# Kernel tuning notes

Measured on AMD Instinct MI355X. Metric: run time of the kernel, lower is better.

## Reference

```python
import jax, jax.numpy as jnp
import numpy as np

NUM_BATCHES = 8  # number of sparse-tensor batch instances


def setup_inputs() -> dict:
    key = jax.random.key(0)
    k1, k2, k3, k4 = jax.random.split(key, 4)
    N, C, R = 262144, 256, 4
    Cr = C // R
    x_feats = jax.random.normal(k1, (N, C), dtype=jnp.float32)
    batch_ids = jax.random.randint(k2, (N,), 0, NUM_BATCHES, dtype=jnp.int32)
    # MinkowskiLinear params (kaiming-ish scale)
    W1 = jax.random.normal(k3, (C, Cr), dtype=jnp.float32) * (1.0 / np.sqrt(C))
    b1 = jnp.zeros((Cr,), dtype=jnp.float32)
    W2 = jax.random.normal(k4, (Cr, C), dtype=jnp.float32) * (1.0 / np.sqrt(Cr))
    b2 = jnp.zeros((C,), dtype=jnp.float32)
    return {"x_feats": x_feats, "batch_ids": batch_ids, "W1": W1, "b1": b1, "W2": W2, "b2": b2}


def reference(x_feats, batch_ids, W1, b1, W2, b2):
    # MinkowskiGlobalPooling: per-batch average over irregular point sets -> [B, C]
    sums = jax.ops.segment_sum(x_feats, batch_ids, num_segments=NUM_BATCHES)
    counts = jax.ops.segment_sum(jnp.ones((x_feats.shape[0],), x_feats.dtype),
                                 batch_ids, num_segments=NUM_BATCHES)
    pooled = sums / jnp.maximum(counts, 1.0)[:, None]  # [B, C]
    # Squeeze-excite MLP: Linear -> ReLU -> Linear -> Sigmoid
    h = jax.nn.relu(pooled @ W1 + b1)                  # [B, C/r]
    y = jax.nn.sigmoid(h @ W2 + b2)                    # [B, C]
    # Broadcast excitation back to each sparse point and multiply
    return y[batch_ids] * x_feats                      # [N, C]
```

## Files before the change

kernel.cpp:

```cpp
#include <hip/hip_runtime.h>
#include <math.h>

#define NB 8
#define C  256
#define CR 64

#define POOL_BLOCKS  1024
#define SCALE_BLOCKS 2048

typedef float vf4 __attribute__((ext_vector_type(4)));

__global__ __launch_bounds__(256) void pool_kernel(
    const float* __restrict__ x,
    const int*   __restrict__ bids,
    float*       __restrict__ partials,
    float*       __restrict__ cpart,
    int N)
{
    __shared__ float lsum[4][NB][C];
    __shared__ float lcnt[4][NB];

    const int tid  = threadIdx.x;
    const int wid  = tid >> 6;
    const int lane = tid & 63;

    vf4   acc[NB];
    float cnt[NB];
    #pragma unroll
    for (int b = 0; b < NB; ++b) { acc[b] = (vf4){0.f,0.f,0.f,0.f}; cnt[b] = 0.f; }

    const int gwave   = blockIdx.x * 4 + wid;
    const int totw    = POOL_BLOCKS * 4;
    const int ngroups = N >> 2;

    for (int g = gwave; g < ngroups; g += totw) {
        const size_t r0 = (size_t)g * 4;
        const int4 bb = *((const int4*)(bids + r0));
        const int b0 = __builtin_amdgcn_readfirstlane(bb.x);
        const int b1 = __builtin_amdgcn_readfirstlane(bb.y);
        const int b2 = __builtin_amdgcn_readfirstlane(bb.z);
        const int b3 = __builtin_amdgcn_readfirstlane(bb.w);
        const vf4 v0 = __builtin_nontemporal_load(((const vf4*)(x + (r0 + 0) * C)) + lane);
        const vf4 v1 = __builtin_nontemporal_load(((const vf4*)(x + (r0 + 1) * C)) + lane);
        const vf4 v2 = __builtin_nontemporal_load(((const vf4*)(x + (r0 + 2) * C)) + lane);
        const vf4 v3 = __builtin_nontemporal_load(((const vf4*)(x + (r0 + 3) * C)) + lane);
        #pragma unroll
        for (int b = 0; b < NB; ++b) {
            const float m0 = (b0 == b) ? 1.f : 0.f;
            const float m1 = (b1 == b) ? 1.f : 0.f;
            const float m2 = (b2 == b) ? 1.f : 0.f;
            const float m3 = (b3 == b) ? 1.f : 0.f;
            acc[b] += v0 * m0;
            acc[b] += v1 * m1;
            acc[b] += v2 * m2;
            acc[b] += v3 * m3;
            cnt[b] += m0 + m1 + m2 + m3;
        }
    }
    if (gwave == 0) {
        for (int row = ngroups * 4; row < N; ++row) {
            const int bb = __builtin_amdgcn_readfirstlane(bids[row]);
            const vf4 v = ((const vf4*)(x + (size_t)row * C))[lane];
            #pragma unroll
            for (int b = 0; b < NB; ++b) {
                const float m = (bb == b) ? 1.f : 0.f;
                acc[b] += v * m;
                cnt[b] += m;
            }
        }
    }

    #pragma unroll
    for (int b = 0; b < NB; ++b)
        ((vf4*)&lsum[wid][b][0])[lane] = acc[b];
    if (lane == 0) {
        #pragma unroll
        for (int b = 0; b < NB; ++b) lcnt[wid][b] = cnt[b];
    }
    __syncthreads();

    float* pout = partials + (size_t)blockIdx.x * (NB * C);
    for (int i = tid; i < NB * C; i += 256)
        pout[i] = lsum[0][0][i] + lsum[1][0][i] + lsum[2][0][i] + lsum[3][0][i];
    if (tid < NB)
        cpart[blockIdx.x * NB + tid] =
            lcnt[0][tid] + lcnt[1][tid] + lcnt[2][tid] + lcnt[3][tid];
}

__global__ __launch_bounds__(256) void reduce_kernel(
    const float* __restrict__ partials,
    const float* __restrict__ cpart,
    float*       __restrict__ partial2,
    float*       __restrict__ c2)
{
    const int jo  = blockIdx.x & 7;
    const int jp  = blockIdx.x >> 3;
    const int col = jo * 256 + threadIdx.x;
    const int PR  = POOL_BLOCKS / 8;

    float s = 0.f;
    #pragma unroll 8
    for (int p = 0; p < PR; ++p)
        s += partials[(size_t)(jp * PR + p) * (NB * C) + col];
    partial2[jp * (NB * C) + col] = s;

    if (jo == 0 && threadIdx.x < NB) {
        float c = 0.f;
        for (int p = 0; p < PR; ++p)
            c += cpart[(jp * PR + p) * NB + threadIdx.x];
        c2[jp * NB + threadIdx.x] = c;
    }
}

__global__ __launch_bounds__(256) void mlp_kernel(
    const float* __restrict__ partial2,
    const float* __restrict__ c2,
    const float* __restrict__ W1,
    const float* __restrict__ b1,
    const float* __restrict__ W2,
    const float* __restrict__ b2,
    float*       __restrict__ y)
{
    __shared__ float pooled[NB][C];
    __shared__ float h[NB][CR];
    __shared__ float cnts[NB];
    const int tid = threadIdx.x;

    if (tid < NB) {
        float c = 0.f;
        #pragma unroll
        for (int j = 0; j < 8; ++j) c += c2[j * NB + tid];
        cnts[tid] = fmaxf(c, 1.f);
    }
    __syncthreads();

    for (int i = tid; i < NB * C; i += 256) {
        float s = 0.f;
        #pragma unroll
        for (int j = 0; j < 8; ++j) s += partial2[j * (NB * C) + i];
        (&pooled[0][0])[i] = s / cnts[i >> 8];
    }
    __syncthreads();

    for (int o = tid; o < NB * CR; o += 256) {
        const int b = o >> 6, j = o & 63;
        float acc = b1[j];
        #pragma unroll 4
        for (int k = 0; k < C; ++k) acc = fmaf(pooled[b][k], W1[k * CR + j], acc);
        (&h[0][0])[o] = fmaxf(acc, 0.f);
    }
    __syncthreads();

    for (int o = tid; o < NB * C; o += 256) {
        const int b = o >> 8, j = o & 255;
        float acc = b2[j];
        #pragma unroll
        for (int k = 0; k < CR; ++k) acc = fmaf(h[b][k], W2[k * C + j], acc);
        y[o] = 1.f / (1.f + __expf(-acc));
    }
}

__global__ __launch_bounds__(256) void scale_kernel(
    const float* __restrict__ x,
    const int*   __restrict__ bids,
    const float* __restrict__ y,
    float*       __restrict__ out,
    int N)
{
    __shared__ float ly[NB][C];
    const int tid = threadIdx.x;
    for (int i = tid; i < NB * C; i += 256) (&ly[0][0])[i] = y[i];
    __syncthreads();

    const int wid  = tid >> 6;
    const int lane = tid & 63;
    const int gwave   = blockIdx.x * 4 + wid;
    const int totw    = SCALE_BLOCKS * 4;
    const int ngroups = N >> 2;

    for (int g = gwave; g < ngroups; g += totw) {
        const size_t r0 = (size_t)g * 4;
        const int4 bb = *((const int4*)(bids + r0));
        const int b0 = __builtin_amdgcn_readfirstlane(bb.x);
        const int b1 = __builtin_amdgcn_readfirstlane(bb.y);
        const int b2 = __builtin_amdgcn_readfirstlane(bb.z);
        const int b3 = __builtin_amdgcn_readfirstlane(bb.w);
        const vf4 v0 = __builtin_nontemporal_load(((const vf4*)(x + (r0 + 0) * C)) + lane);
        const vf4 v1 = __builtin_nontemporal_load(((const vf4*)(x + (r0 + 1) * C)) + lane);
        const vf4 v2 = __builtin_nontemporal_load(((const vf4*)(x + (r0 + 2) * C)) + lane);
        const vf4 v3 = __builtin_nontemporal_load(((const vf4*)(x + (r0 + 3) * C)) + lane);
        const vf4 g0 = ((const vf4*)&ly[b0][0])[lane];
        const vf4 g1 = ((const vf4*)&ly[b1][0])[lane];
        const vf4 g2 = ((const vf4*)&ly[b2][0])[lane];
        const vf4 g3 = ((const vf4*)&ly[b3][0])[lane];
        __builtin_nontemporal_store(v0 * g0, ((vf4*)(out + (r0 + 0) * C)) + lane);
        __builtin_nontemporal_store(v1 * g1, ((vf4*)(out + (r0 + 1) * C)) + lane);
        __builtin_nontemporal_store(v2 * g2, ((vf4*)(out + (r0 + 2) * C)) + lane);
        __builtin_nontemporal_store(v3 * g3, ((vf4*)(out + (r0 + 3) * C)) + lane);
    }
    if (gwave == 0) {
        for (int row = ngroups * 4; row < N; ++row) {
            const int bb = __builtin_amdgcn_readfirstlane(bids[row]);
            const vf4 v  = ((const vf4*)(x + (size_t)row * C))[lane];
            const vf4 gg = ((const vf4*)&ly[bb][0])[lane];
            ((vf4*)(out + (size_t)row * C))[lane] = v * gg;
        }
    }
}

extern "C" void kernel_launch(void* const* d_in, const int* in_sizes, int n_in,
                              void* d_out, int out_size, void* d_ws, size_t ws_size,
                              hipStream_t stream)
{
    const float* x    = (const float*)d_in[0];
    const int*   bids = (const int*)  d_in[1];
    const float* W1   = (const float*)d_in[2];
    const float* b1   = (const float*)d_in[3];
    const float* W2   = (const float*)d_in[4];
    const float* b2   = (const float*)d_in[5];
    float* out = (float*)d_out;

    const int N = in_sizes[1];

    float* partials = (float*)d_ws;
    float* cpart    = partials + POOL_BLOCKS * (NB * C);
    float* partial2 = cpart + POOL_BLOCKS * NB;
    float* c2       = partial2 + 8 * (NB * C);
    float* gy       = c2 + 64;

    pool_kernel  <<<POOL_BLOCKS, 256, 0, stream>>>(x, bids, partials, cpart, N);
    reduce_kernel<<<64, 256, 0, stream>>>(partials, cpart, partial2, c2);
    mlp_kernel   <<<1, 256, 0, stream>>>(partial2, c2, W1, b1, W2, b2, gy);
    scale_kernel <<<SCALE_BLOCKS, 256, 0, stream>>>(x, bids, gy, out, N);
}
```

Before: 169.7 us.

## Fuse partial reduction with MLP per batch, halve pool blocks, widen scale unroll

Result: slower. 174.6 us (+2.9%).

```diff
diff --git a/kernel.cpp b/kernel.cpp
--- a/kernel.cpp
+++ b/kernel.cpp
@@ -5,7 +5,7 @@
 #define C  256
 #define CR 64
 
-#define POOL_BLOCKS  1024
+#define POOL_BLOCKS  512
 #define SCALE_BLOCKS 2048
 
 typedef float vf4 __attribute__((ext_vector_type(4)));
@@ -87,76 +87,54 @@
             lcnt[0][tid] + lcnt[1][tid] + lcnt[2][tid] + lcnt[3][tid];
 }
 
-__global__ __launch_bounds__(256) void reduce_kernel(
+__global__ __launch_bounds__(256) void reduce_mlp_kernel(
     const float* __restrict__ partials,
     const float* __restrict__ cpart,
-    float*       __restrict__ partial2,
-    float*       __restrict__ c2)
-{
-    const int jo  = blockIdx.x & 7;
-    const int jp  = blockIdx.x >> 3;
-    const int col = jo * 256 + threadIdx.x;
-    const int PR  = POOL_BLOCKS / 8;
-
-    float s = 0.f;
-    #pragma unroll 8
-    for (int p = 0; p < PR; ++p)
-        s += partials[(size_t)(jp * PR + p) * (NB * C) + col];
-    partial2[jp * (NB * C) + col] = s;
-
-    if (jo == 0 && threadIdx.x < NB) {
-        float c = 0.f;
-        for (int p = 0; p < PR; ++p)
-            c += cpart[(jp * PR + p) * NB + threadIdx.x];
-        c2[jp * NB + threadIdx.x] = c;
-    }
-}
-
-__global__ __launch_bounds__(256) void mlp_kernel(
-    const float* __restrict__ partial2,
-    const float* __restrict__ c2,
     const float* __restrict__ W1,
     const float* __restrict__ b1,
     const float* __restrict__ W2,
     const float* __restrict__ b2,
     float*       __restrict__ y)
 {
-    __shared__ float pooled[NB][C];
-    __shared__ float h[NB][CR];
-    __shared__ float cnts[NB];
+    __shared__ float pooled[C];
+    __shared__ float h[CR];
+    __shared__ float red[256];
+
+    const int b   = blockIdx.x;
     const int tid = threadIdx.x;
 
-    if (tid < NB) {
-        float c = 0.f;
+    float s = 0.f;
+    #pragma unroll 8
+    for (int p = 0; p < POOL_BLOCKS; ++p)
+        s += partials[(size_t)p * (NB * C) + b * C + tid];
+
+    float c = 0.f;
+    for (int p = tid; p < POOL_BLOCKS; p += 256) c += cpart[p * NB + b];
+    red[tid] = c;
+    __syncthreads();
+    #pragma unroll
+    for (int off = 128; off > 0; off >>= 1) {
+        if (tid < off) red[tid] += red[tid + off];
+        __syncthreads();
+    }
+    const float cnt = fmaxf(red[0], 1.f);
+
+    pooled[tid] = s / cnt;
+    __syncthreads();
+
+    if (tid < CR) {
+        float a = b1[tid];
+        #pragma unroll 4
+        for (int k = 0; k < C; ++k) a = fmaf(pooled[k], W1[k * CR + tid], a);
+        h[tid] = fmaxf(a, 0.f);
+    }
+    __syncthreads();
+
+    {
+        float a = b2[tid];
         #pragma unroll
-        for (int j = 0; j < 8; ++j) c += c2[j * NB + tid];
-        cnts[tid] = fmaxf(c, 1.f);
-    }
-    __syncthreads();
-
-    for (int i = tid; i < NB * C; i += 256) {
-        float s = 0.f;
-        #pragma unroll
-        for (int j = 0; j < 8; ++j) s += partial2[j * (NB * C) + i];
-        (&pooled[0][0])[i] = s / cnts[i >> 8];
-    }
-    __syncthreads();
-
-    for (int o = tid; o < NB * CR; o += 256) {
-        const int b = o >> 6, j = o & 63;
-        float acc = b1[j];
-        #pragma unroll 4
-        for (int k = 0; k < C; ++k) acc = fmaf(pooled[b][k], W1[k * CR + j], acc);
-        (&h[0][0])[o] = fmaxf(acc, 0.f);
-    }
-    __syncthreads();
-
-    for (int o = tid; o < NB * C; o += 256) {
-        const int b = o >> 8, j = o & 255;
-        float acc = b2[j];
-        #pragma unroll
-        for (int k = 0; k < CR; ++k) acc = fmaf(h[b][k], W2[k * C + j], acc);
-        y[o] = 1.f / (1.f + __expf(-acc));
+        for (int k = 0; k < CR; ++k) a = fmaf(h[k], W2[k * C + tid], a);
+        y[b * C + tid] = 1.f / (1.f + __expf(-a));
     }
 }
 
@@ -174,32 +152,49 @@
 
     const int wid  = tid >> 6;
     const int lane = tid & 63;
-    const int gwave   = blockIdx.x * 4 + wid;
-    const int totw    = SCALE_BLOCKS * 4;
-    const int ngroups = N >> 2;
-
-    for (int g = gwave; g < ngroups; g += totw) {
-        const size_t r0 = (size_t)g * 4;
-        const int4 bb = *((const int4*)(bids + r0));
-        const int b0 = __builtin_amdgcn_readfirstlane(bb.x);
-        const int b1 = __builtin_amdgcn_readfirstlane(bb.y);
-        const int b2 = __builtin_amdgcn_readfirstlane(bb.z);
-        const int b3 = __builtin_amdgcn_readfirstlane(bb.w);
+    const int gwave    = blockIdx.x * 4 + wid;
+    const int totw     = SCALE_BLOCKS * 4;
+    const int ngroups8 = N >> 3;
+
+    for (int g = gwave; g < ngroups8; g += totw) {
+        const size_t r0 = (size_t)g * 8;
+        const int4 ba = *((const int4*)(bids + r0));
+        const int4 bc = *((const int4*)(bids + r0 + 4));
+        const int b0 = __builtin_amdgcn_readfirstlane(ba.x);
+        const int b1 = __builtin_amdgcn_readfirstlane(ba.y);
+        const int b2 = __builtin_amdgcn_readfirstlane(ba.z);
+        const int b3 = __builtin_amdgcn_readfirstlane(ba.w);
+        const int b4 = __builtin_amdgcn_readfirstlane(bc.x);
+        const int b5 = __builtin_amdgcn_readfirstlane(bc.y);
+        const int b6 = __builtin_amdgcn_readfirstlane(bc.z);
+        const int b7 = __builtin_amdgcn_readfirstlane(bc.w);
         const vf4 v0 = __builtin_nontemporal_load(((const vf4*)(x + (r0 + 0) * C)) + lane);
         const vf4 v1 = __builtin_nontemporal_load(((const vf4*)(x + (r0 + 1) * C)) + lane);
         const vf4 v2 = __builtin_nontemporal_load(((const vf4*)(x + (r0 + 2) * C)) + lane);
         const vf4 v3 = __builtin_nontemporal_load(((const vf4*)(x + (r0 + 3) * C)) + lane);
+        const vf4 v4 = __builtin_nontemporal_load(((const vf4*)(x + (r0 + 4) * C)) + lane);
+        const vf4 v5 = __builtin_nontemporal_load(((const vf4*)(x + (r0 + 5) * C)) + lane);
+        const vf4 v6 = __builtin_nontemporal_load(((const vf4*)(x + (r0 + 6) * C)) + lane);
+        const vf4 v7 = __builtin_nontemporal_load(((const vf4*)(x + (r0 + 7) * C)) + lane);
         const vf4 g0 = ((const vf4*)&ly[b0][0])[lane];
         const vf4 g1 = ((const vf4*)&ly[b1][0])[lane];
         const vf4 g2 = ((const vf4*)&ly[b2][0])[lane];
         const vf4 g3 = ((const vf4*)&ly[b3][0])[lane];
+        const vf4 g4 = ((const vf4*)&ly[b4][0])[lane];
+        const vf4 g5 = ((const vf4*)&ly[b5][0])[lane];
+        const vf4 g6 = ((const vf4*)&ly[b6][0])[lane];
+        const vf4 g7 = ((const vf4*)&ly[b7][0])[lane];
         __builtin_nontemporal_store(v0 * g0, ((vf4*)(out + (r0 + 0) * C)) + lane);
         __builtin_nontemporal_store(v1 * g1, ((vf4*)(out + (r0 + 1) * C)) + lane);
         __builtin_nontemporal_store(v2 * g2, ((vf4*)(out + (r0 + 2) * C)) + lane);
         __builtin_nontemporal_store(v3 * g3, ((vf4*)(out + (r0 + 3) * C)) + lane);
+        __builtin_nontemporal_store(v4 * g4, ((vf4*)(out + (r0 + 4) * C)) + lane);
+        __builtin_nontemporal_store(v5 * g5, ((vf4*)(out + (r0 + 5) * C)) + lane);
+        __builtin_nontemporal_store(v6 * g6, ((vf4*)(out + (r0 + 6) * C)) + lane);
+        __builtin_nontemporal_store(v7 * g7, ((vf4*)(out + (r0 + 7) * C)) + lane);
     }
     if (gwave == 0) {
-        for (int row = ngroups * 4; row < N; ++row) {
+        for (int row = ngroups8 * 8; row < N; ++row) {
             const int bb = __builtin_amdgcn_readfirstlane(bids[row]);
             const vf4 v  = ((const vf4*)(x + (size_t)row * C))[lane];
             const vf4 gg = ((const vf4*)&ly[bb][0])[lane];
@@ -224,12 +219,9 @@
 
     float* partials = (float*)d_ws;
     float* cpart    = partials + POOL_BLOCKS * (NB * C);
-    float* partial2 = cpart + POOL_BLOCKS * NB;
-    float* c2       = partial2 + 8 * (NB * C);
-    float* gy       = c2 + 64;
-
-    pool_kernel  <<<POOL_BLOCKS, 256, 0, stream>>>(x, bids, partials, cpart, N);
-    reduce_kernel<<<64, 256, 0, stream>>>(partials, cpart, partial2, c2);
-    mlp_kernel   <<<1, 256, 0, stream>>>(partial2, c2, W1, b1, W2, b2, gy);
-    scale_kernel <<<SCALE_BLOCKS, 256, 0, stream>>>(x, bids, gy, out, N);
-}
+    float* gy       = cpart + POOL_BLOCKS * NB;
+
+    pool_kernel      <<<POOL_BLOCKS, 256, 0, stream>>>(x, bids, partials, cpart, N);
+    reduce_mlp_kernel<<<NB, 256, 0, stream>>>(partials, cpart, W1, b1, W2, b2, gy);
+    scale_kernel     <<<SCALE_BLOCKS, 256, 0, stream>>>(x, bids, gy, out, N);
+}
```
